# Kernel tuning notes

Measured on AMD Instinct MI355X. Metric: run time of the kernel, lower is better.

## Reference

```python
import jax, jax.numpy as jnp
import numpy as np

B, HW, N, C, F, ITERS = 32, 4096, 16, 128, 512, 3
EPS_LN = 1e-5
EPS_ATTN = 1e-5


def _ln(x, g, b):
    m = x.mean(-1, keepdims=True)
    v = ((x - m) ** 2).mean(-1, keepdims=True)
    return (x - m) / jnp.sqrt(v + EPS_LN) * g + b


def _gru(x, h, wih, whh, bih, bhh):
    # torch.nn.GRUCell math
    gi = x @ wih.T + bih
    gh = h @ whh.T + bhh
    i_r, i_z, i_n = jnp.split(gi, 3, axis=-1)
    h_r, h_z, h_n = jnp.split(gh, 3, axis=-1)
    r = jax.nn.sigmoid(i_r + h_r)
    z = jax.nn.sigmoid(i_z + h_z)
    n = jnp.tanh(i_n + r * h_n)
    return (1.0 - z) * n + z * h


def setup_inputs() -> dict:
    key = jax.random.key(0)
    ks = jax.random.split(key, 16)
    s = 0.02
    d = {
        'inp': jax.random.normal(ks[0], (B, HW, C), jnp.float32),
        'query': jax.random.normal(ks[1], (B, N, C), jnp.float32),
        'ln_kv_g': jnp.ones((C,), jnp.float32),
        'ln_kv_b': jnp.zeros((C,), jnp.float32),
        'Wk': jax.random.normal(ks[2], (C, C), jnp.float32) * s,
        'Wv': jax.random.normal(ks[3], (C, C), jnp.float32) * s,
        'ln_q_g': jnp.ones((C,), jnp.float32),
        'ln_q_b': jnp.zeros((C,), jnp.float32),
        'Wq': jax.random.normal(ks[4], (C, C), jnp.float32) * s,
        'gru_wih': jax.random.normal(ks[5], (3 * C, C), jnp.float32) * s,
        'gru_whh': jax.random.normal(ks[6], (3 * C, C), jnp.float32) * s,
        'gru_bih': jnp.zeros((3 * C,), jnp.float32),
        'gru_bhh': jnp.zeros((3 * C,), jnp.float32),
        'ln2_g': jnp.ones((C,), jnp.float32),
        'ln2_b': jnp.zeros((C,), jnp.float32),
        'ffn_w1': jax.random.normal(ks[7], (F, C), jnp.float32) * s,
        'ffn_b1': jnp.zeros((F,), jnp.float32),
        'ffn_w2': jax.random.normal(ks[8], (C, F), jnp.float32) * s,
        'ffn_b2': jnp.zeros((C,), jnp.float32),
    }
    return d


def reference(inp, query, ln_kv_g, ln_kv_b, Wk, Wv, ln_q_g, ln_q_b, Wq,
              gru_wih, gru_whh, gru_bih, gru_bhh, ln2_g, ln2_b,
              ffn_w1, ffn_b1, ffn_w2, ffn_b2):
    b, n, c = query.shape
    kv = _ln(inp, ln_kv_g, ln_kv_b)
    k = kv @ Wk.T  # (b, hw, c)
    v = kv @ Wv.T  # (b, hw, c)
    scale = c ** -0.5
    q = query
    a0 = None
    for _ in range(ITERS):
        x = q
        qn = _ln(q, ln_q_g, ln_q_b) @ Wq.T
        logit = jnp.einsum('bqc,bkc->bqk', qn * scale, k)  # (b, n, hw)
        a0 = jax.nn.softmax(logit, axis=1)  # inverted: softmax over slots
        a = a0 / (a0.sum(2, keepdims=True) + EPS_ATTN)  # renorm over keys
        u = jnp.einsum('bqk,bkc->bqc', a, v)
        y = _gru(u.reshape(b * n, c), x.reshape(b * n, c),
                 gru_wih, gru_whh, gru_bih, gru_bhh).reshape(b, n, c)
        z = _ln(y, ln2_g, ln2_b)
        ffn = jax.nn.relu(z @ ffn_w1.T + ffn_b1) @ ffn_w2.T + ffn_b2
        q = y + ffn
    return (q, a0)
```

## Files before the change

kernel.cpp:

```cpp
#include <hip/hip_runtime.h>
#include <math.h>

#define B_ 32
#define HW_ 4096
#define N_ 16
#define C_ 128
#define F_ 512
#define ITERS_ 3
#define EPS_LN 1e-5f
#define EPS_ATTN 1e-5f

typedef __attribute__((ext_vector_type(8))) short short8;
typedef __attribute__((ext_vector_type(4))) float f32x4;

static __device__ __forceinline__ unsigned short f2b(float f) {
    union { float f; unsigned u; } v; v.f = f;
    unsigned r = v.u + 0x7fffu + ((v.u >> 16) & 1u);
    return (unsigned short)(r >> 16);
}
static __device__ __forceinline__ float blo(unsigned u) {
    union { unsigned u; float f; } v; v.u = u << 16; return v.f;
}
static __device__ __forceinline__ float bhi(unsigned u) {
    union { unsigned u; float f; } v; v.u = u & 0xffff0000u; return v.f;
}
static __device__ __forceinline__ void gload_lds16(const void* g, void* l) {
    __builtin_amdgcn_global_load_lds(
        (const __attribute__((address_space(1))) unsigned int*)g,
        (__attribute__((address_space(3))) unsigned int*)l, 16, 0, 0);
}

__global__ __launch_bounds__(256) void k_prep(
    const float* __restrict__ Wk, const float* __restrict__ Wv,
    const float* __restrict__ wih, const float* __restrict__ whh,
    const float* __restrict__ w1, const float* __restrict__ w2,
    unsigned short* __restrict__ Wk_sw, unsigned short* __restrict__ Wv_sw,
    unsigned short* __restrict__ wihT, unsigned short* __restrict__ whhT,
    unsigned short* __restrict__ w1T, unsigned short* __restrict__ w2T,
    const float* __restrict__ query, const float* __restrict__ lnqg,
    const float* __restrict__ lnqb, const float* __restrict__ Wq,
    float* __restrict__ wqTf, unsigned short* __restrict__ qn_g)
{
    __shared__ __align__(16) float xq[16 * 128];
    int tid = threadIdx.x;
    int blk = blockIdx.x;
    if (blk < 32) {
        int t = blk * 256 + tid;
        const float* src; unsigned short* dst; int off;
        if (t < 4096) { src = Wk; dst = Wk_sw; off = t; }
        else          { src = Wv; dst = Wv_sw; off = t - 4096; }
        float4 a = ((const float4*)src)[off];
        uint2 p;
        p.x = (unsigned)f2b(a.x) | ((unsigned)f2b(a.y) << 16);
        p.y = (unsigned)f2b(a.z) | ((unsigned)f2b(a.w) << 16);
        int r = off >> 5;
        int j = off & 31;
        int cg = j >> 1, half = j & 1;
        int dsw = r * 128 + (((cg ^ (r & 7)) << 3)) + (half << 2);
        *(uint2*)(dst + dsw) = p;
        return;
    }
    if (blk < 256) {
        const float* src; unsigned short* dst; int o, g, id, Cin;
        if (blk < 80) {
            id = (blk - 32) * 256 + tid;
            g = id / 384; o = id - g * 384;
            src = wih; dst = wihT; Cin = 128;
        } else if (blk < 128) {
            id = (blk - 80) * 256 + tid;
            g = id / 384; o = id - g * 384;
            src = whh; dst = whhT; Cin = 128;
        } else if (blk < 192) {
            id = (blk - 128) * 256 + tid;
            g = id >> 9; o = id & 511;
            src = w1; dst = w1T; Cin = 128;
        } else {
            id = (blk - 192) * 256 + tid;
            g = id >> 7; o = id & 127;
            src = w2; dst = w2T; Cin = 512;
        }
        float4 a = *(const float4*)(src + o * Cin + g * 4);
        uint2 p;
        p.x = (unsigned)f2b(a.x) | ((unsigned)f2b(a.y) << 16);
        p.y = (unsigned)f2b(a.z) | ((unsigned)f2b(a.w) << 16);
        *(uint2*)(dst + id * 4) = p;
        return;
    }
    if (blk >= 288) {
        int t = (blk - 288) * 256 + tid;
        int c = t & 127, g = t >> 7;
        float4 a = *(const float4*)(Wq + c * 128 + g * 4);
        ((float4*)wqTf)[g * 128 + c] = a;
        return;
    }
    int b = blk - 256;
    int n = tid >> 4, part = tid & 15;
    int row = b * 16 + n;
    const float4* x4 = (const float4*)(query + row * 128 + part * 8);
    float4 x0 = x4[0], x1 = x4[1];
    float s = x0.x + x0.y + x0.z + x0.w + x1.x + x1.y + x1.z + x1.w;
    float ss = x0.x * x0.x + x0.y * x0.y + x0.z * x0.z + x0.w * x0.w +
               x1.x * x1.x + x1.y * x1.y + x1.z * x1.z + x1.w * x1.w;
    s += __shfl_xor(s, 1); s += __shfl_xor(s, 2); s += __shfl_xor(s, 4); s += __shfl_xor(s, 8);
    ss += __shfl_xor(ss, 1); ss += __shfl_xor(ss, 2); ss += __shfl_xor(ss, 4); ss += __shfl_xor(ss, 8);
    float mean = s * (1.f / 128.f);
    float var = ss * (1.f / 128.f) - mean * mean;
    float rstd = rsqrtf(var + EPS_LN);
    const float4* g4 = (const float4*)(lnqg + part * 8);
    const float4* b4 = (const float4*)(lnqb + part * 8);
    float4 g0 = g4[0], g1 = g4[1], bb0 = b4[0], bb1 = b4[1];
    float4 o0, o1;
    o0.x = (x0.x - mean) * rstd * g0.x + bb0.x;
    o0.y = (x0.y - mean) * rstd * g0.y + bb0.y;
    o0.z = (x0.z - mean) * rstd * g0.z + bb0.z;
    o0.w = (x0.w - mean) * rstd * g0.w + bb0.w;
    o1.x = (x1.x - mean) * rstd * g1.x + bb1.x;
    o1.y = (x1.y - mean) * rstd * g1.y + bb1.y;
    o1.z = (x1.z - mean) * rstd * g1.z + bb1.z;
    o1.w = (x1.w - mean) * rstd * g1.w + bb1.w;
    float4* xrow = (float4*)&xq[n * 128];
    xrow[part * 2] = o0;
    xrow[part * 2 + 1] = o1;
    __syncthreads();
    float o[8] = {0.f, 0.f, 0.f, 0.f, 0.f, 0.f, 0.f, 0.f};
    const float4* xv4 = (const float4*)&xq[n * 128];
#pragma unroll 4
    for (int j = 0; j < 32; j++) {
        float4 xv = xv4[j];
#pragma unroll
        for (int i = 0; i < 8; i++) {
            float4 w = ((const float4*)(Wq + (part * 8 + i) * 128))[j];
            o[i] += w.x * xv.x + w.y * xv.y + w.z * xv.z + w.w * xv.w;
        }
    }
    const float scale = 0.08838834764831845f;
#pragma unroll
    for (int i = 0; i < 8; i++)
        qn_g[row * 128 + part * 8 + i] = f2b(o[i] * scale);
}

__global__ __launch_bounds__(512, 4) void k_kvproj(
    const float* __restrict__ inp, const float* __restrict__ lng,
    const float* __restrict__ lnb, const unsigned short* __restrict__ Wk_sw,
    const unsigned short* __restrict__ Wv_sw, unsigned short* __restrict__ Kbf,
    unsigned short* __restrict__ Vt)
{
    __shared__ __align__(16) unsigned short W_lds[128 * 128];
    __shared__ __align__(16) unsigned short T_lds[128 * 132];
    const int tid = threadIdx.x;
    const int wave = tid >> 6, lane = tid & 63;
    const int l15 = lane & 15, q4 = lane >> 4;
    const int kof = q4 * 8;
    const int tile0 = blockIdx.x * 128;
    const int b = tile0 >> 12;
    const int hwbase = tile0 & (HW_ - 1);

    {
        const char* gw = (const char*)Wk_sw + wave * 4096 + lane * 16;
        char* lw = (char*)W_lds + wave * 4096;
#pragma unroll
        for (int j = 0; j < 4; j++)
            gload_lds16(gw + j * 1024, lw + j * 1024);
    }

    float x[4][8];
    {
        const float* rowp = inp + (tile0 + (wave << 4) + l15) * C_;
        float s = 0.f, ss = 0.f;
#pragma unroll
        for (int ks = 0; ks < 4; ks++) {
#pragma unroll
            for (int h = 0; h < 2; h++) {
                float4 v = *(const float4*)(rowp + ks * 32 + kof + h * 4);
                x[ks][h * 4 + 0] = v.x; x[ks][h * 4 + 1] = v.y;
                x[ks][h * 4 + 2] = v.z; x[ks][h * 4 + 3] = v.w;
                s += v.x + v.y + v.z + v.w;
                ss += v.x * v.x + v.y * v.y + v.z * v.z + v.w * v.w;
            }
        }
        s += __shfl_xor(s, 16);  s += __shfl_xor(s, 32);
        ss += __shfl_xor(ss, 16); ss += __shfl_xor(ss, 32);
        float mean = s * (1.f / 128.f);
        float var = ss * (1.f / 128.f) - mean * mean;
        float rstd = rsqrtf(var + EPS_LN);
#pragma unroll
        for (int ks = 0; ks < 4; ks++) {
#pragma unroll
            for (int h = 0; h < 2; h++) {
                float4 g = *(const float4*)(lng + ks * 32 + kof + h * 4);
                float4 bb = *(const float4*)(lnb + ks * 32 + kof + h * 4);
                x[ks][h * 4 + 0] = (x[ks][h * 4 + 0] - mean) * rstd * g.x + bb.x;
                x[ks][h * 4 + 1] = (x[ks][h * 4 + 1] - mean) * rstd * g.y + bb.y;
                x[ks][h * 4 + 2] = (x[ks][h * 4 + 2] - mean) * rstd * g.z + bb.z;
                x[ks][h * 4 + 3] = (x[ks][h * 4 + 3] - mean) * rstd * g.w + bb.w;
            }
        }
    }
    short8 af[4];
#pragma unroll
    for (int ks = 0; ks < 4; ks++) {
        union { short8 s8; unsigned u[4]; } p;
#pragma unroll
        for (int j = 0; j < 4; j++)
            p.u[j] = (unsigned)f2b(x[ks][2 * j]) | ((unsigned)f2b(x[ks][2 * j + 1]) << 16);
        af[ks] = p.s8;
    }

    __syncthreads();

    f32x4 acc[8];
#pragma unroll
    for (int nt = 0; nt < 8; nt++) {
        acc[nt] = (f32x4){0.f, 0.f, 0.f, 0.f};
#pragma unroll
        for (int ks = 0; ks < 4; ks++) {
            short8 bf = *(const short8*)&W_lds[(nt * 16 + l15) * 128 + ((ks * 4 + q4) ^ (l15 & 7)) * 8];
            acc[nt] = __builtin_amdgcn_mfma_f32_16x16x32_bf16(af[ks], bf, acc[nt], 0, 0, 0);
        }
    }
#pragma unroll
    for (int nt = 0; nt < 8; nt++) {
        int c = nt * 16 + l15;
#pragma unroll
        for (int i = 0; i < 4; i++)
            T_lds[((wave << 4) + (q4 << 2) + i) * 132 + c] = f2b(acc[nt][i]);
    }
    __syncthreads();

    {
        int row = tid >> 2, part = tid & 3;
        uint4* dst = (uint4*)&Kbf[(b * HW_ + hwbase + row) * C_ + part * 32];
#pragma unroll
        for (int j = 0; j < 4; j++)
            dst[j] = *(const uint4*)&T_lds[row * 132 + part * 32 + j * 8];
    }
    {
        const char* gw = (const char*)Wv_sw + wave * 4096 + lane * 16;
        char* lw = (char*)W_lds + wave * 4096;
#pragma unroll
        for (int j = 0; j < 4; j++)
            gload_lds16(gw + j * 1024, lw + j * 1024);
    }
    __syncthreads();

#pragma unroll
    for (int nt = 0; nt < 8; nt++) {
        acc[nt] = (f32x4){0.f, 0.f, 0.f, 0.f};
#pragma unroll
        for (int ks = 0; ks < 4; ks++) {
            short8 bf = *(const short8*)&W_lds[(nt * 16 + l15) * 128 + ((ks * 4 + q4) ^ (l15 & 7)) * 8];
            acc[nt] = __builtin_amdgcn_mfma_f32_16x16x32_bf16(af[ks], bf, acc[nt], 0, 0, 0);
        }
    }
#pragma unroll
    for (int nt = 0; nt < 8; nt++) {
        int c = nt * 16 + l15;
#pragma unroll
        for (int i = 0; i < 4; i++)
            T_lds[c * 132 + (wave << 4) + (q4 << 2) + i] = f2b(acc[nt][i]);
    }
    __syncthreads();

    {
        int c = tid >> 2, part = tid & 3;
        uint4* dst = (uint4*)&Vt[(b * C_ + c) * HW_ + hwbase + part * 32];
#pragma unroll
        for (int j = 0; j < 4; j++)
            dst[j] = *(const uint4*)&T_lds[c * 132 + part * 32 + j * 8];
    }
}

__global__ __launch_bounds__(256) void k_attn(
    const unsigned short* __restrict__ qn_g, const unsigned short* __restrict__ Kbf,
    const unsigned short* __restrict__ Vt, float* __restrict__ Upart,
    float* __restrict__ rspart, float* __restrict__ a0_out, int last)
{
    __shared__ __align__(16) float Ul[4][16 * 132];
    __shared__ __align__(16) unsigned short Pb[4][16 * 40];
    __shared__ float rsw[4][16];
    const int b = blockIdx.y, chunk = blockIdx.x;
    const int tid = threadIdx.x;
    const int wave = tid >> 6, lane = tid & 63;
    const int l15 = lane & 15, q4 = lane >> 4;
    const int kof = q4 * 8;
    const int hwb = chunk * 128 + wave * 32;

    short8 aq[4];
#pragma unroll
    for (int ks = 0; ks < 4; ks++)
        aq[ks] = *(const short8*)&qn_g[(b * 16 + l15) * 128 + ks * 32 + kof];
    short8 av[8];
#pragma unroll
    for (int ct = 0; ct < 8; ct++)
        av[ct] = *(const short8*)&Vt[(b * C_ + ct * 16 + l15) * HW_ + hwb + kof];

    unsigned short* Pw = &Pb[wave][0];
    float rs[4] = {0.f, 0.f, 0.f, 0.f};
#pragma unroll
    for (int s = 0; s < 2; s++) {
        int hwt = hwb + s * 16;
        f32x4 sa = {0.f, 0.f, 0.f, 0.f};
#pragma unroll
        for (int ks = 0; ks < 4; ks++) {
            short8 bk = *(const short8*)&Kbf[(b * HW_ + hwt + l15) * C_ + ks * 32 + kof];
            sa = __builtin_amdgcn_mfma_f32_16x16x32_bf16(aq[ks], bk, sa, 0, 0, 0);
        }
        float mx = fmaxf(fmaxf(sa[0], sa[1]), fmaxf(sa[2], sa[3]));
        mx = fmaxf(mx, __shfl_xor(mx, 16));
        mx = fmaxf(mx, __shfl_xor(mx, 32));
        float e[4]; float ssum = 0.f;
#pragma unroll
        for (int i = 0; i < 4; i++) { e[i] = __expf(sa[i] - mx); ssum += e[i]; }
        ssum += __shfl_xor(ssum, 16);
        ssum += __shfl_xor(ssum, 32);
        float inv = 1.f / ssum;
#pragma unroll
        for (int i = 0; i < 4; i++) {
            float a0v = e[i] * inv;
            rs[i] += a0v;
            if (last) a0_out[(b * 16 + q4 * 4 + i) * HW_ + hwt + l15] = a0v;
            Pw[(q4 * 4 + i) * 40 + s * 16 + l15] = f2b(a0v);
        }
    }
#pragma unroll
    for (int i = 0; i < 4; i++) {
        rs[i] += __shfl_xor(rs[i], 1);
        rs[i] += __shfl_xor(rs[i], 2);
        rs[i] += __shfl_xor(rs[i], 4);
        rs[i] += __shfl_xor(rs[i], 8);
    }
    if (l15 == 0) {
#pragma unroll
        for (int i = 0; i < 4; i++) rsw[wave][q4 * 4 + i] = rs[i];
    }
    short8 bp = *(const short8*)&Pw[l15 * 40 + kof];
#pragma unroll
    for (int ct = 0; ct < 8; ct++) {
        f32x4 ua = __builtin_amdgcn_mfma_f32_16x16x32_bf16(av[ct], bp, (f32x4){0.f, 0.f, 0.f, 0.f}, 0, 0, 0);
        *(f32x4*)&Ul[wave][l15 * 132 + ct * 16 + (q4 << 2)] = ua;
    }
    __syncthreads();
    {
        float* up = Upart + (b * 32 + chunk) * 2048;
#pragma unroll
        for (int k = 0; k < 8; k++) {
            int idx = tid + k * 256;
            int q = idx >> 7, c = idx & 127;
            up[idx] = Ul[0][q * 132 + c] + Ul[1][q * 132 + c] +
                      Ul[2][q * 132 + c] + Ul[3][q * 132 + c];
        }
        if (tid < 16)
            rspart[(b * 32 + chunk) * 16 + tid] =
                rsw[0][tid] + rsw[1][tid] + rsw[2][tid] + rsw[3][tid];
    }
}

__global__ __launch_bounds__(1024, 4) void k_tail(
    const float* __restrict__ Upart, const float* __restrict__ rspart,
    const float* __restrict__ hsrc, float* __restrict__ q_buf,
    const unsigned short* __restrict__ wihT, const unsigned short* __restrict__ whhT,
    const float* __restrict__ bih, const float* __restrict__ bhh,
    const float* __restrict__ ln2g, const float* __restrict__ ln2b,
    const unsigned short* __restrict__ w1T, const float* __restrict__ b1,
    const unsigned short* __restrict__ w2T, const float* __restrict__ b2,
    const float* __restrict__ lnqg, const float* __restrict__ lnqb,
    const float* __restrict__ wqTf, unsigned short* __restrict__ qn_g,
    float* __restrict__ out_q, int last)
{
    __shared__ __align__(16) float red[1024];
    __shared__ __align__(16) float u_l[128];
    __shared__ __align__(16) float h_l[128];
    __shared__ __align__(16) float y_l[128];
    __shared__ __align__(16) float z_l[128];
    __shared__ __align__(16) float g_l[768];
    __shared__ __align__(16) float h1_l[512];
    __shared__ float srs;
    const int tid = threadIdx.x;
    const int row = blockIdx.x;
    const int b = row >> 4, q = row & 15;

    {
        int c = tid & 127, h = tid >> 7;
        const float* up = Upart + (b * 32 + h * 4) * 2048 + q * 128 + c;
        float part = 0.f;
#pragma unroll
        for (int ch = 0; ch < 4; ch++) part += up[ch * 2048];
        red[tid] = part;
        if (tid < 128) h_l[tid] = hsrc[row * 128 + tid];
        if (tid >= 128 && tid < 160) {
            int t = tid - 128;
            float v = rspart[(b * 32 + t) * 16 + q];
            v += __shfl_xor(v, 1); v += __shfl_xor(v, 2); v += __shfl_xor(v, 4);
            v += __shfl_xor(v, 8); v += __shfl_xor(v, 16);
            if (t == 0) srs = v;
        }
    }
    __syncthreads();
    if (tid < 128) {
        float s = 0.f;
#pragma unroll
        for (int h = 0; h < 8; h++) s += red[tid + 128 * h];
        u_l[tid] = s / (srs + EPS_ATTN);
    }
    __syncthreads();
    if (tid < 768) {
        int o = tid;
        const uint2* wp;
        const float* src;
        float bias;
        if (o < 384) { wp = (const uint2*)wihT + o; src = u_l; bias = bih[o]; }
        else         { wp = (const uint2*)whhT + (o - 384); src = h_l; bias = bhh[o - 384]; }
        float acc = 0.f;
#pragma unroll 4
        for (int g = 0; g < 32; g++) {
            uint2 w = wp[g * 384];
            float4 sv = *(const float4*)&src[g * 4];
            acc += blo(w.x) * sv.x + bhi(w.x) * sv.y
                 + blo(w.y) * sv.z + bhi(w.y) * sv.w;
        }
        g_l[o] = acc + bias;
    }
    __syncthreads();
    if (tid < 128) {
        int c = tid;
        float ir = g_l[c], iz = g_l[128 + c], in_ = g_l[256 + c];
        float hr = g_l[384 + c], hz = g_l[512 + c], hn = g_l[640 + c];
        float rr = 1.f / (1.f + expf(-(ir + hr)));
        float zz = 1.f / (1.f + expf(-(iz + hz)));
        float nn = tanhf(in_ + rr * hn);
        y_l[c] = (1.f - zz) * nn + zz * h_l[c];
    }
    __syncthreads();
    {
        int l = tid & 63;
        float v0 = y_l[l], v1 = y_l[l + 64];
        float s = v0 + v1, ss = v0 * v0 + v1 * v1;
#pragma unroll
        for (int off = 1; off < 64; off <<= 1) {
            s += __shfl_xor(s, off);
            ss += __shfl_xor(ss, off);
        }
        float mean = s * (1.f / 128.f);
        float var = ss * (1.f / 128.f) - mean * mean;
        float rstd = rsqrtf(var + EPS_LN);
        if (tid < 128)
            z_l[tid] = (y_l[tid] - mean) * rstd * ln2g[tid] + ln2b[tid];
    }
    __syncthreads();
    {
        int f = tid & 511, hh = tid >> 9;
        const uint2* wp = (const uint2*)w1T + f;
        float acc = 0.f;
#pragma unroll 4
        for (int j = 0; j < 16; j++) {
            int g = hh * 16 + j;
            uint2 w = wp[g * 512];
            float4 zv = *(const float4*)&z_l[g * 4];
            acc += blo(w.x) * zv.x + bhi(w.x) * zv.y
                 + blo(w.y) * zv.z + bhi(w.y) * zv.w;
        }
        red[tid] = acc;
    }
    __syncthreads();
    if (tid < 512)
        h1_l[tid] = fmaxf(red[tid] + red[tid + 512] + b1[tid], 0.f);
    __syncthreads();
    {
        int c = tid & 127, h8 = tid >> 7;
        const uint2* wp = (const uint2*)w2T + c;
        float acc = 0.f;
#pragma unroll 4
        for (int j = 0; j < 16; j++) {
            int g = h8 * 16 + j;
            uint2 w = wp[g * 128];
            float4 hv = *(const float4*)&h1_l[g * 4];
            acc += blo(w.x) * hv.x + bhi(w.x) * hv.y
                 + blo(w.y) * hv.z + bhi(w.y) * hv.w;
        }
        red[tid] = acc;
    }
    __syncthreads();
    if (tid < 128) {
        float f2 = 0.f;
#pragma unroll
        for (int k = 0; k < 8; k++) f2 += red[tid + 128 * k];
        float qn = y_l[tid] + f2 + b2[tid];
        u_l[tid] = qn;
        q_buf[row * 128 + tid] = qn;
        if (last) out_q[row * 128 + tid] = qn;
    }
    if (last) return;
    __syncthreads();
    {
        int l = tid & 63;
        float v0 = u_l[l], v1 = u_l[l + 64];
        float s = v0 + v1, ss = v0 * v0 + v1 * v1;
#pragma unroll
        for (int off = 1; off < 64; off <<= 1) {
            s += __shfl_xor(s, off);
            ss += __shfl_xor(ss, off);
        }
        float mean = s * (1.f / 128.f);
        float var = ss * (1.f / 128.f) - mean * mean;
        float rstd = rsqrtf(var + EPS_LN);
        if (tid < 128)
            z_l[tid] = (u_l[tid] - mean) * rstd * lnqg[tid] + lnqb[tid];
    }
    __syncthreads();
    {
        int c = tid & 127, h8 = tid >> 7;
        const float4* wp = (const float4*)wqTf + c;
        float acc = 0.f;
#pragma unroll
        for (int j = 0; j < 4; j++) {
            int g = h8 * 4 + j;
            float4 w = wp[g * 128];
            float4 zv = *(const float4*)&z_l[g * 4];
            acc += w.x * zv.x + w.y * zv.y + w.z * zv.z + w.w * zv.w;
        }
        red[tid] = acc;
    }
    __syncthreads();
    if (tid < 128) {
        float qa = 0.f;
#pragma unroll
        for (int k = 0; k < 8; k++) qa += red[tid + 128 * k];
        qn_g[row * 128 + tid] = f2b(qa * 0.08838834764831845f);
    }
}

extern "C" void kernel_launch(void* const* d_in, const int* in_sizes, int n_in,
                              void* d_out, int out_size, void* d_ws, size_t ws_size,
                              hipStream_t stream) {
    const float* inp     = (const float*)d_in[0];
    const float* query   = (const float*)d_in[1];
    const float* ln_kv_g = (const float*)d_in[2];
    const float* ln_kv_b = (const float*)d_in[3];
    const float* Wk      = (const float*)d_in[4];
    const float* Wv      = (const float*)d_in[5];
    const float* ln_q_g  = (const float*)d_in[6];
    const float* ln_q_b  = (const float*)d_in[7];
    const float* Wq      = (const float*)d_in[8];
    const float* gru_wih = (const float*)d_in[9];
    const float* gru_whh = (const float*)d_in[10];
    const float* gru_bih = (const float*)d_in[11];
    const float* gru_bhh = (const float*)d_in[12];
    const float* ln2_g   = (const float*)d_in[13];
    const float* ln2_b   = (const float*)d_in[14];
    const float* ffn_w1  = (const float*)d_in[15];
    const float* ffn_b1  = (const float*)d_in[16];
    const float* ffn_w2  = (const float*)d_in[17];
    const float* ffn_b2  = (const float*)d_in[18];

    char* ws = (char*)d_ws;
    unsigned short* Kbf    = (unsigned short*)ws;
    unsigned short* Vt     = (unsigned short*)(ws + 33554432);
    float* q_buf           = (float*)(ws + 67108864);
    float* Upart           = (float*)(ws + 67371008);
    float* rspart          = (float*)(ws + 75759616);
    unsigned short* qn_g   = (unsigned short*)(ws + 75825152);
    unsigned short* Wk_sw  = (unsigned short*)(ws + 75956224);
    unsigned short* Wv_sw  = (unsigned short*)(ws + 75988992);
    unsigned short* wihT   = (unsigned short*)(ws + 76021760);
    unsigned short* whhT   = (unsigned short*)(ws + 76120064);
    unsigned short* w1T    = (unsigned short*)(ws + 76218368);
    unsigned short* w2T    = (unsigned short*)(ws + 76349440);
    float* wqTf            = (float*)(ws + 76480512);

    float* out_q  = (float*)d_out;
    float* out_a0 = out_q + B_ * N_ * C_;

    k_prep<<<dim3(304), dim3(256), 0, stream>>>(
        Wk, Wv, gru_wih, gru_whh, ffn_w1, ffn_w2,
        Wk_sw, Wv_sw, wihT, whhT, w1T, w2T,
        query, ln_q_g, ln_q_b, Wq, wqTf, qn_g);
    k_kvproj<<<dim3((B_ * HW_) / 128), dim3(512), 0, stream>>>(
        inp, ln_kv_g, ln_kv_b, Wk_sw, Wv_sw, Kbf, Vt);

    for (int it = 0; it < ITERS_; it++) {
        int last = (it == ITERS_ - 1) ? 1 : 0;
        const float* hsrc = (it == 0) ? query : q_buf;
        k_attn<<<dim3(32, B_), dim3(256), 0, stream>>>(
            qn_g, Kbf, Vt, Upart, rspart, out_a0, last);
        k_tail<<<dim3(B_ * N_), dim3(1024), 0, stream>>>(
            Upart, rspart, hsrc, q_buf, wihT, whhT, gru_bih, gru_bhh,
            ln2_g, ln2_b, w1T, ffn_b1, w2T, ffn_b2,
            ln_q_g, ln_q_b, wqTf, qn_g, out_q, last);
    }
}
```

Measured before the change: 287.1 us.

## Process two slot rows per k_tail block to share weight loads

k_tail now handles two consecutive (batch, slot) rows per block with 512 threads instead of one row per block with 1024 threads. Each bf16 weight element loaded for the GRU, FFN and Wq matvecs is applied to both rows, which halves weight traffic per row and halves the grid size. The cost is more serial work per thread, fewer blocks (256) to fill the GPU, and doubled LDS buffers.

```diff
diff --git a/kernel.cpp b/kernel.cpp
--- a/kernel.cpp
+++ b/kernel.cpp
@@ -355,7 +355,7 @@
     }
 }
 
-__global__ __launch_bounds__(1024, 4) void k_tail(
+__global__ __launch_bounds__(512) void k_tail(
     const float* __restrict__ Upart, const float* __restrict__ rspart,
     const float* __restrict__ hsrc, float* __restrict__ q_buf,
     const unsigned short* __restrict__ wihT, const unsigned short* __restrict__ whhT,
@@ -367,73 +367,107 @@
     const float* __restrict__ wqTf, unsigned short* __restrict__ qn_g,
     float* __restrict__ out_q, int last)
 {
-    __shared__ __align__(16) float red[1024];
-    __shared__ __align__(16) float u_l[128];
-    __shared__ __align__(16) float h_l[128];
-    __shared__ __align__(16) float y_l[128];
-    __shared__ __align__(16) float z_l[128];
-    __shared__ __align__(16) float g_l[768];
-    __shared__ __align__(16) float h1_l[512];
-    __shared__ float srs;
+    __shared__ __align__(16) float red0[512], red1[512];
+    __shared__ __align__(16) float u0_l[128], u1_l[128];
+    __shared__ __align__(16) float h0_l[128], h1_l[128];
+    __shared__ __align__(16) float y0_l[128], y1_l[128];
+    __shared__ __align__(16) float z0_l[128], z1_l[128];
+    __shared__ __align__(16) float g0_l[768], g1_l[768];
+    __shared__ __align__(16) float f0_l[512], f1_l[512];
+    __shared__ float srs0, srs1;
     const int tid = threadIdx.x;
-    const int row = blockIdx.x;
-    const int b = row >> 4, q = row & 15;
+    const int row0 = blockIdx.x * 2, row1 = row0 + 1;
+    const int b = row0 >> 4, q0 = row0 & 15;
 
     {
         int c = tid & 127, h = tid >> 7;
-        const float* up = Upart + (b * 32 + h * 4) * 2048 + q * 128 + c;
-        float part = 0.f;
-#pragma unroll
-        for (int ch = 0; ch < 4; ch++) part += up[ch * 2048];
-        red[tid] = part;
-        if (tid < 128) h_l[tid] = hsrc[row * 128 + tid];
-        if (tid >= 128 && tid < 160) {
-            int t = tid - 128;
-            float v = rspart[(b * 32 + t) * 16 + q];
+        const float* upA = Upart + (b * 32 + h * 8) * 2048 + q0 * 128 + c;
+        float a = 0.f, bv = 0.f;
+#pragma unroll
+        for (int ch = 0; ch < 8; ch++) {
+            a  += upA[ch * 2048];
+            bv += upA[ch * 2048 + 128];
+        }
+        red0[tid] = a; red1[tid] = bv;
+        if (tid < 128) h0_l[tid] = hsrc[row0 * 128 + tid];
+        else if (tid < 256) h1_l[tid - 128] = hsrc[row1 * 128 + (tid - 128)];
+        if (tid >= 256 && tid < 288) {
+            int t = tid - 256;
+            float v = rspart[(b * 32 + t) * 16 + q0];
             v += __shfl_xor(v, 1); v += __shfl_xor(v, 2); v += __shfl_xor(v, 4);
             v += __shfl_xor(v, 8); v += __shfl_xor(v, 16);
-            if (t == 0) srs = v;
+            if (t == 0) srs0 = v;
+        }
+        if (tid >= 320 && tid < 352) {
+            int t = tid - 320;
+            float v = rspart[(b * 32 + t) * 16 + q0 + 1];
+            v += __shfl_xor(v, 1); v += __shfl_xor(v, 2); v += __shfl_xor(v, 4);
+            v += __shfl_xor(v, 8); v += __shfl_xor(v, 16);
+            if (t == 0) srs1 = v;
         }
     }
     __syncthreads();
     if (tid < 128) {
-        float s = 0.f;
-#pragma unroll
-        for (int h = 0; h < 8; h++) s += red[tid + 128 * h];
-        u_l[tid] = s / (srs + EPS_ATTN);
-    }
-    __syncthreads();
-    if (tid < 768) {
+        float s = red0[tid] + red0[tid + 128] + red0[tid + 256] + red0[tid + 384];
+        u0_l[tid] = s / (srs0 + EPS_ATTN);
+    } else if (tid < 256) {
+        int c = tid - 128;
+        float s = red1[c] + red1[c + 128] + red1[c + 256] + red1[c + 384];
+        u1_l[c] = s / (srs1 + EPS_ATTN);
+    }
+    __syncthreads();
+    {
         int o = tid;
-        const uint2* wp;
-        const float* src;
-        float bias;
-        if (o < 384) { wp = (const uint2*)wihT + o; src = u_l; bias = bih[o]; }
-        else         { wp = (const uint2*)whhT + (o - 384); src = h_l; bias = bhh[o - 384]; }
-        float acc = 0.f;
+        const uint2* wp; const float *sA, *sB; float bias;
+        if (o < 384) { wp = (const uint2*)wihT + o; sA = u0_l; sB = u1_l; bias = bih[o]; }
+        else         { wp = (const uint2*)whhT + (o - 384); sA = h0_l; sB = h1_l; bias = bhh[o - 384]; }
+        float fa = 0.f, fb = 0.f;
 #pragma unroll 4
         for (int g = 0; g < 32; g++) {
             uint2 w = wp[g * 384];
-            float4 sv = *(const float4*)&src[g * 4];
-            acc += blo(w.x) * sv.x + bhi(w.x) * sv.y
-                 + blo(w.y) * sv.z + bhi(w.y) * sv.w;
-        }
-        g_l[o] = acc + bias;
-    }
-    __syncthreads();
-    if (tid < 128) {
-        int c = tid;
-        float ir = g_l[c], iz = g_l[128 + c], in_ = g_l[256 + c];
-        float hr = g_l[384 + c], hz = g_l[512 + c], hn = g_l[640 + c];
+            float4 a4 = *(const float4*)&sA[g * 4];
+            float4 b4 = *(const float4*)&sB[g * 4];
+            float w0 = blo(w.x), w1v = bhi(w.x), w2v = blo(w.y), w3 = bhi(w.y);
+            fa += w0 * a4.x + w1v * a4.y + w2v * a4.z + w3 * a4.w;
+            fb += w0 * b4.x + w1v * b4.y + w2v * b4.z + w3 * b4.w;
+        }
+        g0_l[o] = fa + bias; g1_l[o] = fb + bias;
+        if (tid < 256) {
+            int o2 = tid + 512;
+            const uint2* wp2 = (const uint2*)whhT + (o2 - 384);
+            float fa2 = 0.f, fb2 = 0.f;
+#pragma unroll 4
+            for (int g = 0; g < 32; g++) {
+                uint2 w = wp2[g * 384];
+                float4 a4 = *(const float4*)&h0_l[g * 4];
+                float4 b4 = *(const float4*)&h1_l[g * 4];
+                float w0 = blo(w.x), w1v = bhi(w.x), w2v = blo(w.y), w3 = bhi(w.y);
+                fa2 += w0 * a4.x + w1v * a4.y + w2v * a4.z + w3 * a4.w;
+                fb2 += w0 * b4.x + w1v * b4.y + w2v * b4.z + w3 * b4.w;
+            }
+            float bias2 = bhh[o2 - 384];
+            g0_l[o2] = fa2 + bias2; g1_l[o2] = fb2 + bias2;
+        }
+    }
+    __syncthreads();
+    if (tid < 256) {
+        int c = tid & 127, r = tid >> 7;
+        const float* gl = r ? g1_l : g0_l;
+        const float* hl = r ? h1_l : h0_l;
+        float* yl = r ? y1_l : y0_l;
+        float ir = gl[c], iz = gl[128 + c], in_ = gl[256 + c];
+        float hr = gl[384 + c], hz = gl[512 + c], hn = gl[640 + c];
         float rr = 1.f / (1.f + expf(-(ir + hr)));
         float zz = 1.f / (1.f + expf(-(iz + hz)));
         float nn = tanhf(in_ + rr * hn);
-        y_l[c] = (1.f - zz) * nn + zz * h_l[c];
-    }
-    __syncthreads();
-    {
+        yl[c] = (1.f - zz) * nn + zz * hl[c];
+    }
+    __syncthreads();
+    {
+        int r = tid >> 8;
+        const float* yl = r ? y1_l : y0_l;
         int l = tid & 63;
-        float v0 = y_l[l], v1 = y_l[l + 64];
+        float v0 = yl[l], v1 = yl[l + 64];
         float s = v0 + v1, ss = v0 * v0 + v1 * v1;
 #pragma unroll
         for (int off = 1; off < 64; off <<= 1) {
@@ -443,57 +477,68 @@
         float mean = s * (1.f / 128.f);
         float var = ss * (1.f / 128.f) - mean * mean;
         float rstd = rsqrtf(var + EPS_LN);
-        if (tid < 128)
-            z_l[tid] = (y_l[tid] - mean) * rstd * ln2g[tid] + ln2b[tid];
-    }
-    __syncthreads();
-    {
-        int f = tid & 511, hh = tid >> 9;
-        const uint2* wp = (const uint2*)w1T + f;
-        float acc = 0.f;
+        int c = tid & 255;
+        if (c < 128) {
+            float* zl = r ? z1_l : z0_l;
+            zl[c] = (yl[c] - mean) * rstd * ln2g[c] + ln2b[c];
+        }
+    }
+    __syncthreads();
+    {
+        const uint2* wp = (const uint2*)w1T + tid;
+        float fa = 0.f, fb = 0.f;
 #pragma unroll 4
-        for (int j = 0; j < 16; j++) {
-            int g = hh * 16 + j;
+        for (int g = 0; g < 32; g++) {
             uint2 w = wp[g * 512];
-            float4 zv = *(const float4*)&z_l[g * 4];
-            acc += blo(w.x) * zv.x + bhi(w.x) * zv.y
-                 + blo(w.y) * zv.z + bhi(w.y) * zv.w;
-        }
-        red[tid] = acc;
-    }
-    __syncthreads();
-    if (tid < 512)
-        h1_l[tid] = fmaxf(red[tid] + red[tid + 512] + b1[tid], 0.f);
-    __syncthreads();
-    {
-        int c = tid & 127, h8 = tid >> 7;
+            float4 za = *(const float4*)&z0_l[g * 4];
+            float4 zb = *(const float4*)&z1_l[g * 4];
+            float w0 = blo(w.x), w1v = bhi(w.x), w2v = blo(w.y), w3 = bhi(w.y);
+            fa += w0 * za.x + w1v * za.y + w2v * za.z + w3 * za.w;
+            fb += w0 * zb.x + w1v * zb.y + w2v * zb.z + w3 * zb.w;
+        }
+        float bb = b1[tid];
+        f0_l[tid] = fmaxf(fa + bb, 0.f);
+        f1_l[tid] = fmaxf(fb + bb, 0.f);
+    }
+    __syncthreads();
+    {
+        int c = tid & 127, k4 = tid >> 7;
         const uint2* wp = (const uint2*)w2T + c;
-        float acc = 0.f;
+        float fa = 0.f, fb = 0.f;
 #pragma unroll 4
-        for (int j = 0; j < 16; j++) {
-            int g = h8 * 16 + j;
+        for (int j = 0; j < 32; j++) {
+            int g = k4 * 32 + j;
             uint2 w = wp[g * 128];
-            float4 hv = *(const float4*)&h1_l[g * 4];
-            acc += blo(w.x) * hv.x + bhi(w.x) * hv.y
-                 + blo(w.y) * hv.z + bhi(w.y) * hv.w;
-        }
-        red[tid] = acc;
+            float4 ha = *(const float4*)&f0_l[g * 4];
+            float4 hb = *(const float4*)&f1_l[g * 4];
+            float w0 = blo(w.x), w1v = bhi(w.x), w2v = blo(w.y), w3 = bhi(w.y);
+            fa += w0 * ha.x + w1v * ha.y + w2v * ha.z + w3 * ha.w;
+            fb += w0 * hb.x + w1v * hb.y + w2v * hb.z + w3 * hb.w;
+        }
+        red0[tid] = fa; red1[tid] = fb;
     }
     __syncthreads();
     if (tid < 128) {
-        float f2 = 0.f;
-#pragma unroll
-        for (int k = 0; k < 8; k++) f2 += red[tid + 128 * k];
-        float qn = y_l[tid] + f2 + b2[tid];
-        u_l[tid] = qn;
-        q_buf[row * 128 + tid] = qn;
-        if (last) out_q[row * 128 + tid] = qn;
+        float f2 = red0[tid] + red0[tid + 128] + red0[tid + 256] + red0[tid + 384];
+        float qn = y0_l[tid] + f2 + b2[tid];
+        u0_l[tid] = qn;
+        q_buf[row0 * 128 + tid] = qn;
+        if (last) out_q[row0 * 128 + tid] = qn;
+    } else if (tid < 256) {
+        int c = tid - 128;
+        float f2 = red1[c] + red1[c + 128] + red1[c + 256] + red1[c + 384];
+        float qn = y1_l[c] + f2 + b2[c];
+        u1_l[c] = qn;
+        q_buf[row1 * 128 + c] = qn;
+        if (last) out_q[row1 * 128 + c] = qn;
     }
     if (last) return;
     __syncthreads();
     {
+        int r = tid >> 8;
+        const float* yl = r ? u1_l : u0_l;
         int l = tid & 63;
-        float v0 = u_l[l], v1 = u_l[l + 64];
+        float v0 = yl[l], v1 = yl[l + 64];
         float s = v0 + v1, ss = v0 * v0 + v1 * v1;
 #pragma unroll
         for (int off = 1; off < 64; off <<= 1) {
@@ -503,29 +548,36 @@
         float mean = s * (1.f / 128.f);
         float var = ss * (1.f / 128.f) - mean * mean;
         float rstd = rsqrtf(var + EPS_LN);
-        if (tid < 128)
-            z_l[tid] = (u_l[tid] - mean) * rstd * lnqg[tid] + lnqb[tid];
-    }
-    __syncthreads();
-    {
-        int c = tid & 127, h8 = tid >> 7;
+        int c = tid & 255;
+        if (c < 128) {
+            float* zl = r ? z1_l : z0_l;
+            zl[c] = (yl[c] - mean) * rstd * lnqg[c] + lnqb[c];
+        }
+    }
+    __syncthreads();
+    {
+        int c = tid & 127, k4 = tid >> 7;
         const float4* wp = (const float4*)wqTf + c;
-        float acc = 0.f;
-#pragma unroll
-        for (int j = 0; j < 4; j++) {
-            int g = h8 * 4 + j;
+        float fa = 0.f, fb = 0.f;
+#pragma unroll
+        for (int j = 0; j < 8; j++) {
+            int g = k4 * 8 + j;
             float4 w = wp[g * 128];
-            float4 zv = *(const float4*)&z_l[g * 4];
-            acc += w.x * zv.x + w.y * zv.y + w.z * zv.z + w.w * zv.w;
-        }
-        red[tid] = acc;
+            float4 za = *(const float4*)&z0_l[g * 4];
+            float4 zb = *(const float4*)&z1_l[g * 4];
+            fa += w.x * za.x + w.y * za.y + w.z * za.z + w.w * za.w;
+            fb += w.x * zb.x + w.y * zb.y + w.z * zb.z + w.w * zb.w;
+        }
+        red0[tid] = fa; red1[tid] = fb;
     }
     __syncthreads();
     if (tid < 128) {
-        float qa = 0.f;
-#pragma unroll
-        for (int k = 0; k < 8; k++) qa += red[tid + 128 * k];
-        qn_g[row * 128 + tid] = f2b(qa * 0.08838834764831845f);
+        float qa = red0[tid] + red0[tid + 128] + red0[tid + 256] + red0[tid + 384];
+        qn_g[row0 * 128 + tid] = f2b(qa * 0.08838834764831845f);
+    } else if (tid < 256) {
+        int c = tid - 128;
+        float qa = red1[c] + red1[c + 128] + red1[c + 256] + red1[c + 384];
+        qn_g[row1 * 128 + c] = f2b(qa * 0.08838834764831845f);
     }
 }
 
@@ -582,7 +634,7 @@
         const float* hsrc = (it == 0) ? query : q_buf;
         k_attn<<<dim3(32, B_), dim3(256), 0, stream>>>(
             qn_g, Kbf, Vt, Upart, rspart, out_a0, last);
-        k_tail<<<dim3(B_ * N_), dim3(1024), 0, stream>>>(
+        k_tail<<<dim3((B_ * N_) / 2), dim3(512), 0, stream>>>(
             Upart, rspart, hsrc, q_buf, wihT, whhT, gru_bih, gru_bhh,
             ln2_g, ln2_b, w1T, ffn_b1, w2T, ffn_b2,
             ln_q_g, ln_q_b, wqTf, qn_g, out_q, last);
```

New measurement: 282.8 us. No clear change (-1.5%).
